# Kernel tuning notes

Measured on AMD Instinct MI355X. Metric: run time of the kernel, lower is better.

Reference implementation:

```python
import jax, jax.numpy as jnp
import numpy as np

B, A, D, H = 2048, 32, 128, 256

def setup_inputs() -> dict:
    key = jax.random.key(0)
    ks = jax.random.split(key, 12)
    s = lambda fan_in: 1.0 / np.sqrt(fan_in)
    return {
        "obs": jax.random.normal(ks[0], (B, A, D), dtype=jnp.float32),
        "act": jax.random.normal(ks[1], (B, A, 8), dtype=jnp.float32),
        "enc_W": jax.random.uniform(ks[2], (H, D), jnp.float32, -s(D), s(D)),
        "enc_b": jax.random.uniform(ks[3], (H,), jnp.float32, -s(D), s(D)),
        "fobs_W": jax.random.uniform(ks[4], (H, H), jnp.float32, -s(H), s(H)),
        "fobs_b": jax.random.uniform(ks[5], (H,), jnp.float32, -s(H), s(H)),
        "W_ih": jax.random.uniform(ks[6], (3 * H, H), jnp.float32, -s(H), s(H)),
        "b_ih": jax.random.uniform(ks[7], (3 * H,), jnp.float32, -s(H), s(H)),
        "W_hh": jax.random.uniform(ks[8], (3 * H, H), jnp.float32, -s(H), s(H)),
        "b_hh": jax.random.uniform(ks[9], (3 * H,), jnp.float32, -s(H), s(H)),
        "dec_W": jax.random.uniform(ks[10], (1, H), jnp.float32, -s(H), s(H)),
        "dec_b": jax.random.uniform(ks[11], (1,), jnp.float32, -s(H), s(H)),
    }

def _gru_cell(x, h, W_ih, b_ih, W_hh, b_hh):
    # torch.nn.GRUCell: gates stacked as [reset, update, new]
    gi = x @ W_ih.T + b_ih          # [N, 3H]
    gh = h @ W_hh.T + b_hh          # [N, 3H]
    i_r, i_z, i_n = jnp.split(gi, 3, axis=-1)
    h_r, h_z, h_n = jnp.split(gh, 3, axis=-1)
    r = jax.nn.sigmoid(i_r + h_r)
    z = jax.nn.sigmoid(i_z + h_z)
    n = jnp.tanh(i_n + r * h_n)
    return (1.0 - z) * n + z * h

def reference(obs, act, enc_W, enc_b, fobs_W, fobs_b, W_ih, b_ih, W_hh, b_hh, dec_W, dec_b):
    b, a, d = obs.shape
    x = obs.reshape(b * a, d)                         # [B*A, D]
    e = jax.nn.relu(x @ enc_W.T + enc_b)              # encoder + ReLU
    h = e @ fobs_W.T + fobs_b                         # h_out
    # k = 0: comm input is zeros
    h = _gru_cell(jnp.zeros_like(h), h, W_ih, b_ih, W_hh, b_hh)
    # k = 1: masked mean over other agents == (sum_j h_j - h_i) / n_agents
    hA = h.reshape(b, a, -1)                          # [B, A, H]
    c = (hA.sum(axis=1, keepdims=True) - hA) / a      # [B, A, H]
    h = _gru_cell(c.reshape(b * a, -1), h, W_ih, b_ih, W_hh, b_hh)
    return (h @ dec_W.T + dec_b).reshape(b, a, -1)    # [B, A, 1]
```

## Files before the change

### kernel.cpp

```cpp
#include <hip/hip_runtime.h>
#include <hip/hip_fp16.h>


#define NB   2048
#define NA   32
#define DIN  128
#define HID  256
#define SA   264
#define MROWS 64

typedef _Float16 half8  __attribute__((ext_vector_type(8)));
typedef float    float4v __attribute__((ext_vector_type(4)));

#define ENC_OFF    0
#define FOBS_OFF   32768
#define WIH_OFF    98304
#define WHH_OFF    294912
#define PREP_TOTAL 491520

__global__ void prep_weights(const float* __restrict__ encW, const float* __restrict__ fobsW,
                             const float* __restrict__ wih,  const float* __restrict__ whh,
                             _Float16* __restrict__ prep) {
    int F = blockIdx.x * 256 + threadIdx.x;
    if (F >= PREP_TOTAL) return;
    const float* src; int K, NT, local = F;
    if (F < FOBS_OFF)     { src = encW;  K = 128; NT = 16; }
    else if (F < WIH_OFF) { src = fobsW; K = 256; NT = 16; local = F - FOBS_OFF; }
    else if (F < WHH_OFF) { src = wih;   K = 256; NT = 48; local = F - WIH_OFF; }
    else                  { src = whh;   K = 256; NT = 48; local = F - WHH_OFF; }
    int j    = local & 7;
    int lane = (local >> 3) & 63;
    int t    = local >> 9;
    int nt   = t % NT;
    int ks   = t / NT;
    int col  = nt * 16 + (lane & 15);
    int k    = ks * 32 + ((lane >> 4) << 3) + j;
    prep[F] = (_Float16)src[col * K + k];
}

__device__ __forceinline__ float sigmoid_f(float x) {
    return 1.f / (1.f + __expf(-x));
}
__device__ __forceinline__ float tanh_f(float x) {
    return 1.f - 2.f / (__expf(2.f * x) + 1.f);
}

__device__ __forceinline__ half8 ldB(const _Float16* __restrict__ prepm, int NT, int nt, int ks,
                                     const float* __restrict__ raw, int K, int use_prep, int lane) {
    if (use_prep)
        return *(const half8*)(prepm + (((ks * NT + nt) * 64 + lane) << 3));
    half8 b;
    int l16 = lane & 15, kq = (lane >> 4) << 3;
    #pragma unroll
    for (int j = 0; j < 8; j++)
        b[j] = (_Float16)raw[(nt * 16 + l16) * K + ks * 32 + kq + j];
    return b;
}

__global__ __launch_bounds__(1024) void commnet_fused(
    const float* __restrict__ obs, const _Float16* __restrict__ prep,
    const float* __restrict__ enc_b, const float* __restrict__ fobs_b,
    const float* __restrict__ b_ih, const float* __restrict__ b_hh,
    const float* __restrict__ dec_W, const float* __restrict__ dec_b,
    float* __restrict__ out,
    const float* __restrict__ encW, const float* __restrict__ fobsW,
    const float* __restrict__ wih, const float* __restrict__ whh,
    int use_prep)
{
    const int b    = blockIdx.x;
    const int tid  = threadIdx.x;
    const int lane = tid & 63;
    const int nt   = tid >> 6;
    const int l16  = lane & 15;
    const int quad = lane >> 4;
    const int kq   = quad << 3;
    const int col  = nt * 16 + l16;

    __shared__ __align__(16) _Float16 sA[2][MROWS * SA];
    __shared__ __align__(16) float S[2][HID];
    __shared__ float Srow[MROWS];

    {
        const float* obsb = obs + (size_t)b * MROWS * DIN;
        int r   = tid >> 4;
        int off = (tid & 15) << 3;
        const float* src = obsb + r * DIN + off;
        float4v v0 = *(const float4v*)(src);
        float4v v1 = *(const float4v*)(src + 4);
        half8 hv;
        hv[0] = (_Float16)v0[0]; hv[1] = (_Float16)v0[1];
        hv[2] = (_Float16)v0[2]; hv[3] = (_Float16)v0[3];
        hv[4] = (_Float16)v1[0]; hv[5] = (_Float16)v1[1];
        hv[6] = (_Float16)v1[2]; hv[7] = (_Float16)v1[3];
        *(half8*)(&sA[0][r * SA + off]) = hv;
    }
    __syncthreads();

    {
        float4v acc[4];
        float4v z = {0.f, 0.f, 0.f, 0.f};
        acc[0] = z; acc[1] = z; acc[2] = z; acc[3] = z;
        #pragma unroll
        for (int ks = 0; ks < 4; ks++) {
            int kbase = ks * 32 + kq;
            half8 Af[4];
            #pragma unroll
            for (int mt = 0; mt < 4; mt++)
                Af[mt] = *(const half8*)(&sA[0][(mt * 16 + l16) * SA + kbase]);
            half8 b0 = ldB(prep + ENC_OFF, 16, nt, ks, encW, DIN, use_prep, lane);
            #pragma unroll
            for (int mt = 0; mt < 4; mt++)
                acc[mt] = __builtin_amdgcn_mfma_f32_16x16x32_f16(Af[mt], b0, acc[mt], 0, 0, 0);
        }
        float bb = enc_b[col];
        #pragma unroll
        for (int mt = 0; mt < 4; mt++)
            #pragma unroll
            for (int r = 0; r < 4; r++) {
                int row = mt * 16 + quad * 4 + r;
                sA[1][row * SA + col] = (_Float16)fmaxf(acc[mt][r] + bb, 0.f);
            }
    }
    __syncthreads();

    float4v hacc[4];
    {
        float4v z = {0.f, 0.f, 0.f, 0.f};
        hacc[0] = z; hacc[1] = z; hacc[2] = z; hacc[3] = z;
        #pragma unroll 2
        for (int ks = 0; ks < 8; ks++) {
            int kbase = ks * 32 + kq;
            half8 Af[4];
            #pragma unroll
            for (int mt = 0; mt < 4; mt++)
                Af[mt] = *(const half8*)(&sA[1][(mt * 16 + l16) * SA + kbase]);
            half8 b0 = ldB(prep + FOBS_OFF, 16, nt, ks, fobsW, HID, use_prep, lane);
            #pragma unroll
            for (int mt = 0; mt < 4; mt++)
                hacc[mt] = __builtin_amdgcn_mfma_f32_16x16x32_f16(Af[mt], b0, hacc[mt], 0, 0, 0);
        }
        float bb = fobs_b[col];
        #pragma unroll
        for (int mt = 0; mt < 4; mt++)
            #pragma unroll
            for (int r = 0; r < 4; r++) {
                int row = mt * 16 + quad * 4 + r;
                float h = hacc[mt][r] + bb;
                hacc[mt][r] = h;
                sA[0][row * SA + col] = (_Float16)h;
            }
    }
    __syncthreads();

    #pragma unroll 1
    for (int half = 0; half < 2; half++) {
        const int rb = half * 32;
        float4v aR[2], aZ[2], aN[2];
        float4v z = {0.f, 0.f, 0.f, 0.f};
        aR[0] = z; aR[1] = z; aZ[0] = z; aZ[1] = z; aN[0] = z; aN[1] = z;
        #pragma unroll 2
        for (int ks = 0; ks < 8; ks++) {
            const int kbase = ks * 32 + kq;
            half8 A0 = *(const half8*)(&sA[0][(rb + l16) * SA + kbase]);
            half8 A1 = *(const half8*)(&sA[0][(rb + 16 + l16) * SA + kbase]);
            half8 bR = ldB(prep + WHH_OFF, 48,  0 + nt, ks, whh, HID, use_prep, lane);
            half8 bZ = ldB(prep + WHH_OFF, 48, 16 + nt, ks, whh, HID, use_prep, lane);
            half8 bN = ldB(prep + WHH_OFF, 48, 32 + nt, ks, whh, HID, use_prep, lane);
            aR[0] = __builtin_amdgcn_mfma_f32_16x16x32_f16(A0, bR, aR[0], 0, 0, 0);
            aR[1] = __builtin_amdgcn_mfma_f32_16x16x32_f16(A1, bR, aR[1], 0, 0, 0);
            aZ[0] = __builtin_amdgcn_mfma_f32_16x16x32_f16(A0, bZ, aZ[0], 0, 0, 0);
            aZ[1] = __builtin_amdgcn_mfma_f32_16x16x32_f16(A1, bZ, aZ[1], 0, 0, 0);
            aN[0] = __builtin_amdgcn_mfma_f32_16x16x32_f16(A0, bN, aN[0], 0, 0, 0);
            aN[1] = __builtin_amdgcn_mfma_f32_16x16x32_f16(A1, bN, aN[1], 0, 0, 0);
        }
        float biR = b_ih[col],       bhR = b_hh[col];
        float biZ = b_ih[256 + col], bhZ = b_hh[256 + col];
        float biN = b_ih[512 + col], bhN = b_hh[512 + col];
        float psum = 0.f;
        #pragma unroll
        for (int mt = 0; mt < 2; mt++)
            #pragma unroll
            for (int r = 0; r < 4; r++) {
                int row = rb + mt * 16 + quad * 4 + r;
                float rg = sigmoid_f(biR + aR[mt][r] + bhR);
                float zg = sigmoid_f(biZ + aZ[mt][r] + bhZ);
                float ng = tanh_f(biN + rg * (aN[mt][r] + bhN));
                float hold = hacc[half * 2 + mt][r];
                float h1 = (1.f - zg) * ng + zg * hold;
                sA[1][row * SA + col] = (_Float16)h1;
                psum += h1;
            }
        psum += __shfl_xor(psum, 16);
        psum += __shfl_xor(psum, 32);
        if (lane < 16) S[half][nt * 16 + lane] = psum;
    }
    __syncthreads();

    {
        #pragma unroll
        for (int it = 0; it < 2; it++) {
            int i  = tid + it * 1024;
            int r  = i >> 5;
            int c8 = (i & 31) << 3;
            const float* Sp = &S[r >> 5][0];
            half8 hv = *(const half8*)(&sA[1][r * SA + c8]);
            float4v t0 = *(const float4v*)(Sp + c8);
            float4v t1 = *(const float4v*)(Sp + c8 + 4);
            half8 cv;
            cv[0] = (_Float16)((t0[0] - (float)hv[0]) * (1.f / 32.f));
            cv[1] = (_Float16)((t0[1] - (float)hv[1]) * (1.f / 32.f));
            cv[2] = (_Float16)((t0[2] - (float)hv[2]) * (1.f / 32.f));
            cv[3] = (_Float16)((t0[3] - (float)hv[3]) * (1.f / 32.f));
            cv[4] = (_Float16)((t1[0] - (float)hv[4]) * (1.f / 32.f));
            cv[5] = (_Float16)((t1[1] - (float)hv[5]) * (1.f / 32.f));
            cv[6] = (_Float16)((t1[2] - (float)hv[6]) * (1.f / 32.f));
            cv[7] = (_Float16)((t1[3] - (float)hv[7]) * (1.f / 32.f));
            *(half8*)(&sA[0][r * SA + c8]) = cv;
        }
        if (tid < MROWS) Srow[tid] = 0.f;
    }
    __syncthreads();

    #pragma unroll 1
    for (int half = 0; half < 2; half++) {
        const int rb = half * 32;
        float4v aR[2], aZ[2], aNi[2], aNh[2];
        float4v z = {0.f, 0.f, 0.f, 0.f};
        aR[0] = z; aR[1] = z; aZ[0] = z; aZ[1] = z;
        aNi[0] = z; aNi[1] = z; aNh[0] = z; aNh[1] = z;
        #pragma unroll 1
        for (int ks = 0; ks < 8; ks++) {
            const int kbase = ks * 32 + kq;
            {
                half8 C0 = *(const half8*)(&sA[0][(rb + l16) * SA + kbase]);
                half8 C1 = *(const half8*)(&sA[0][(rb + 16 + l16) * SA + kbase]);
                half8 bR = ldB(prep + WIH_OFF, 48,  0 + nt, ks, wih, HID, use_prep, lane);
                half8 bZ = ldB(prep + WIH_OFF, 48, 16 + nt, ks, wih, HID, use_prep, lane);
                half8 bN = ldB(prep + WIH_OFF, 48, 32 + nt, ks, wih, HID, use_prep, lane);
                aR[0]  = __builtin_amdgcn_mfma_f32_16x16x32_f16(C0, bR, aR[0], 0, 0, 0);
                aR[1]  = __builtin_amdgcn_mfma_f32_16x16x32_f16(C1, bR, aR[1], 0, 0, 0);
                aZ[0]  = __builtin_amdgcn_mfma_f32_16x16x32_f16(C0, bZ, aZ[0], 0, 0, 0);
                aZ[1]  = __builtin_amdgcn_mfma_f32_16x16x32_f16(C1, bZ, aZ[1], 0, 0, 0);
                aNi[0] = __builtin_amdgcn_mfma_f32_16x16x32_f16(C0, bN, aNi[0], 0, 0, 0);
                aNi[1] = __builtin_amdgcn_mfma_f32_16x16x32_f16(C1, bN, aNi[1], 0, 0, 0);
            }
            {
                half8 H0 = *(const half8*)(&sA[1][(rb + l16) * SA + kbase]);
                half8 H1 = *(const half8*)(&sA[1][(rb + 16 + l16) * SA + kbase]);
                half8 bR = ldB(prep + WHH_OFF, 48,  0 + nt, ks, whh, HID, use_prep, lane);
                half8 bZ = ldB(prep + WHH_OFF, 48, 16 + nt, ks, whh, HID, use_prep, lane);
                half8 bN = ldB(prep + WHH_OFF, 48, 32 + nt, ks, whh, HID, use_prep, lane);
                aR[0]  = __builtin_amdgcn_mfma_f32_16x16x32_f16(H0, bR, aR[0], 0, 0, 0);
                aR[1]  = __builtin_amdgcn_mfma_f32_16x16x32_f16(H1, bR, aR[1], 0, 0, 0);
                aZ[0]  = __builtin_amdgcn_mfma_f32_16x16x32_f16(H0, bZ, aZ[0], 0, 0, 0);
                aZ[1]  = __builtin_amdgcn_mfma_f32_16x16x32_f16(H1, bZ, aZ[1], 0, 0, 0);
                aNh[0] = __builtin_amdgcn_mfma_f32_16x16x32_f16(H0, bN, aNh[0], 0, 0, 0);
                aNh[1] = __builtin_amdgcn_mfma_f32_16x16x32_f16(H1, bN, aNh[1], 0, 0, 0);
            }
        }

        float biR = b_ih[col],       bhR = b_hh[col];
        float biZ = b_ih[256 + col], bhZ = b_hh[256 + col];
        float biN = b_ih[512 + col], bhN = b_hh[512 + col];
        float dw  = dec_W[col];
        float p[2][4];
        #pragma unroll
        for (int mt = 0; mt < 2; mt++)
            #pragma unroll
            for (int r = 0; r < 4; r++) {
                int row = rb + mt * 16 + quad * 4 + r;
                float rg = sigmoid_f(aR[mt][r] + biR + bhR);
                float zg = sigmoid_f(aZ[mt][r] + biZ + bhZ);
                float ng = tanh_f((aNi[mt][r] + biN) + rg * (aNh[mt][r] + bhN));
                float h1v = (float)sA[1][row * SA + col];
                float h2 = (1.f - zg) * ng + zg * h1v;
                p[mt][r] = h2 * dw;
            }
        #pragma unroll
        for (int m = 1; m <= 8; m <<= 1) {
            #pragma unroll
            for (int mt = 0; mt < 2; mt++)
                #pragma unroll
                for (int r = 0; r < 4; r++)
                    p[mt][r] += __shfl_xor(p[mt][r], m);
        }
        if (l16 == 0) {
            #pragma unroll
            for (int mt = 0; mt < 2; mt++)
                #pragma unroll
                for (int r = 0; r < 4; r++)
                    atomicAdd(&Srow[rb + mt * 16 + quad * 4 + r], p[mt][r]);
        }
    }
    __syncthreads();
    if (tid < MROWS) out[(size_t)b * MROWS + tid] = Srow[tid] + dec_b[0];
}

extern "C" void kernel_launch(void* const* d_in, const int* in_sizes, int n_in,
                              void* d_out, int out_size, void* d_ws, size_t ws_size,
                              hipStream_t stream) {
    const float* obs   = (const float*)d_in[0];
    const float* encW  = (const float*)d_in[2];
    const float* encb  = (const float*)d_in[3];
    const float* fobsW = (const float*)d_in[4];
    const float* fobsb = (const float*)d_in[5];
    const float* wih   = (const float*)d_in[6];
    const float* bih   = (const float*)d_in[7];
    const float* whh   = (const float*)d_in[8];
    const float* bhh   = (const float*)d_in[9];
    const float* decW  = (const float*)d_in[10];
    const float* decb  = (const float*)d_in[11];
    float* out = (float*)d_out;

    _Float16* prep = (_Float16*)d_ws;
    int use_prep = (ws_size >= (size_t)PREP_TOTAL * sizeof(_Float16)) ? 1 : 0;
    if (use_prep) {
        prep_weights<<<(PREP_TOTAL + 255) / 256, 256, 0, stream>>>(encW, fobsW, wih, whh, prep);
    }
    commnet_fused<<<NB / 2, 1024, 0, stream>>>(obs, prep, encb, fobsb, bih, bhh, decW, decb, out,
                                               encW, fobsW, wih, whh, use_prep);
}
```

Baseline: 236.6 us.

## Fold mean-field comm into combined GRU weights to drop second-step input GEMM

```diff
diff --git a/kernel.cpp b/kernel.cpp
--- a/kernel.cpp
+++ b/kernel.cpp
@@ -14,8 +14,9 @@
 
 #define ENC_OFF    0
 #define FOBS_OFF   32768
-#define WIH_OFF    98304
-#define WHH_OFF    294912
+#define WIHN_OFF   98304
+#define WHH_OFF    163840
+#define COMB_OFF   360448
 #define PREP_TOTAL 491520
 
 __global__ void prep_weights(const float* __restrict__ encW, const float* __restrict__ fobsW,
@@ -23,19 +24,25 @@
                              _Float16* __restrict__ prep) {
     int F = blockIdx.x * 256 + threadIdx.x;
     if (F >= PREP_TOTAL) return;
-    const float* src; int K, NT, local = F;
-    if (F < FOBS_OFF)     { src = encW;  K = 128; NT = 16; }
-    else if (F < WIH_OFF) { src = fobsW; K = 256; NT = 16; local = F - FOBS_OFF; }
-    else if (F < WHH_OFF) { src = wih;   K = 256; NT = 48; local = F - WIH_OFF; }
-    else                  { src = whh;   K = 256; NT = 48; local = F - WHH_OFF; }
+    const float* srcA; const float* srcB = nullptr;
+    int K, NT, local, rowoff = 0; float scA = 1.f, scB = 0.f;
+    if (F < FOBS_OFF)      { srcA = encW;  K = 128; NT = 16; local = F; }
+    else if (F < WIHN_OFF) { srcA = fobsW; K = 256; NT = 16; local = F - FOBS_OFF; }
+    else if (F < WHH_OFF)  { srcA = wih;   K = 256; NT = 16; local = F - WIHN_OFF;
+                             rowoff = 512; scA = -0.03125f; }
+    else if (F < COMB_OFF) { srcA = whh;   K = 256; NT = 48; local = F - WHH_OFF; }
+    else                   { srcA = whh; srcB = wih; K = 256; NT = 32;
+                             local = F - COMB_OFF; scB = -0.03125f; }
     int j    = local & 7;
     int lane = (local >> 3) & 63;
     int t    = local >> 9;
     int nt   = t % NT;
     int ks   = t / NT;
-    int col  = nt * 16 + (lane & 15);
+    int row  = rowoff + nt * 16 + (lane & 15);
     int k    = ks * 32 + ((lane >> 4) << 3) + j;
-    prep[F] = (_Float16)src[col * K + k];
+    float v  = srcA[row * K + k] * scA;
+    if (srcB) v += srcB[row * K + k] * scB;
+    prep[F] = (_Float16)v;
 }
 
 __device__ __forceinline__ float sigmoid_f(float x) {
@@ -46,14 +53,20 @@
 }
 
 __device__ __forceinline__ half8 ldB(const _Float16* __restrict__ prepm, int NT, int nt, int ks,
-                                     const float* __restrict__ raw, int K, int use_prep, int lane) {
-    if (use_prep)
-        return *(const half8*)(prepm + (((ks * NT + nt) * 64 + lane) << 3));
-    half8 b;
-    int l16 = lane & 15, kq = (lane >> 4) << 3;
+                                     int lane) {
+    return *(const half8*)(prepm + (((ks * NT + nt) * 64 + lane) << 3));
+}
+__device__ __forceinline__ half8 ldBraw(const float* __restrict__ rawA, float scA,
+                                        const float* __restrict__ rawB, float scB,
+                                        int rowoff, int K, int nt, int ks, int lane) {
+    half8 b; int l16 = lane & 15, kq = (lane >> 4) << 3;
+    int row = rowoff + nt * 16 + l16;
     #pragma unroll
-    for (int j = 0; j < 8; j++)
-        b[j] = (_Float16)raw[(nt * 16 + l16) * K + ks * 32 + kq + j];
+    for (int j = 0; j < 8; j++) {
+        float v = rawA[row * K + ks * 32 + kq + j] * scA;
+        if (rawB) v += rawB[row * K + ks * 32 + kq + j] * scB;
+        b[j] = (_Float16)v;
+    }
     return b;
 }
 
@@ -77,7 +90,8 @@
     const int col  = nt * 16 + l16;
 
     __shared__ __align__(16) _Float16 sA[2][MROWS * SA];
-    __shared__ __align__(16) float S[2][HID];
+    __shared__ __align__(16) float Scol[2][HID];
+    __shared__ __align__(16) float ep[2][3 * HID];
     __shared__ float Srow[MROWS];
 
     {
@@ -107,7 +121,8 @@
             #pragma unroll
             for (int mt = 0; mt < 4; mt++)
                 Af[mt] = *(const half8*)(&sA[0][(mt * 16 + l16) * SA + kbase]);
-            half8 b0 = ldB(prep + ENC_OFF, 16, nt, ks, encW, DIN, use_prep, lane);
+            half8 b0 = use_prep ? ldB(prep + ENC_OFF, 16, nt, ks, lane)
+                                : ldBraw(encW, 1.f, nullptr, 0.f, 0, DIN, nt, ks, lane);
             #pragma unroll
             for (int mt = 0; mt < 4; mt++)
                 acc[mt] = __builtin_amdgcn_mfma_f32_16x16x32_f16(Af[mt], b0, acc[mt], 0, 0, 0);
@@ -134,7 +149,8 @@
             #pragma unroll
             for (int mt = 0; mt < 4; mt++)
                 Af[mt] = *(const half8*)(&sA[1][(mt * 16 + l16) * SA + kbase]);
-            half8 b0 = ldB(prep + FOBS_OFF, 16, nt, ks, fobsW, HID, use_prep, lane);
+            half8 b0 = use_prep ? ldB(prep + FOBS_OFF, 16, nt, ks, lane)
+                                : ldBraw(fobsW, 1.f, nullptr, 0.f, 0, HID, nt, ks, lane);
             #pragma unroll
             for (int mt = 0; mt < 4; mt++)
                 hacc[mt] = __builtin_amdgcn_mfma_f32_16x16x32_f16(Af[mt], b0, hacc[mt], 0, 0, 0);
@@ -163,9 +179,12 @@
             const int kbase = ks * 32 + kq;
             half8 A0 = *(const half8*)(&sA[0][(rb + l16) * SA + kbase]);
             half8 A1 = *(const half8*)(&sA[0][(rb + 16 + l16) * SA + kbase]);
-            half8 bR = ldB(prep + WHH_OFF, 48,  0 + nt, ks, whh, HID, use_prep, lane);
-            half8 bZ = ldB(prep + WHH_OFF, 48, 16 + nt, ks, whh, HID, use_prep, lane);
-            half8 bN = ldB(prep + WHH_OFF, 48, 32 + nt, ks, whh, HID, use_prep, lane);
+            half8 bR = use_prep ? ldB(prep + WHH_OFF, 48,  0 + nt, ks, lane)
+                                : ldBraw(whh, 1.f, nullptr, 0.f, 0, HID,  0 + nt, ks, lane);
+            half8 bZ = use_prep ? ldB(prep + WHH_OFF, 48, 16 + nt, ks, lane)
+                                : ldBraw(whh, 1.f, nullptr, 0.f, 0, HID, 16 + nt, ks, lane);
+            half8 bN = use_prep ? ldB(prep + WHH_OFF, 48, 32 + nt, ks, lane)
+                                : ldBraw(whh, 1.f, nullptr, 0.f, 0, HID, 32 + nt, ks, lane);
             aR[0] = __builtin_amdgcn_mfma_f32_16x16x32_f16(A0, bR, aR[0], 0, 0, 0);
             aR[1] = __builtin_amdgcn_mfma_f32_16x16x32_f16(A1, bR, aR[1], 0, 0, 0);
             aZ[0] = __builtin_amdgcn_mfma_f32_16x16x32_f16(A0, bZ, aZ[0], 0, 0, 0);
@@ -192,30 +211,57 @@
             }
         psum += __shfl_xor(psum, 16);
         psum += __shfl_xor(psum, 32);
-        if (lane < 16) S[half][nt * 16 + lane] = psum;
+        if (lane < 16) Scol[half][nt * 16 + lane] = psum;
     }
     __syncthreads();
 
     {
-        #pragma unroll
-        for (int it = 0; it < 2; it++) {
-            int i  = tid + it * 1024;
-            int r  = i >> 5;
-            int c8 = (i & 31) << 3;
-            const float* Sp = &S[r >> 5][0];
-            half8 hv = *(const half8*)(&sA[1][r * SA + c8]);
-            float4v t0 = *(const float4v*)(Sp + c8);
-            float4v t1 = *(const float4v*)(Sp + c8 + 4);
-            half8 cv;
-            cv[0] = (_Float16)((t0[0] - (float)hv[0]) * (1.f / 32.f));
-            cv[1] = (_Float16)((t0[1] - (float)hv[1]) * (1.f / 32.f));
-            cv[2] = (_Float16)((t0[2] - (float)hv[2]) * (1.f / 32.f));
-            cv[3] = (_Float16)((t0[3] - (float)hv[3]) * (1.f / 32.f));
-            cv[4] = (_Float16)((t1[0] - (float)hv[4]) * (1.f / 32.f));
-            cv[5] = (_Float16)((t1[1] - (float)hv[5]) * (1.f / 32.f));
-            cv[6] = (_Float16)((t1[2] - (float)hv[6]) * (1.f / 32.f));
-            cv[7] = (_Float16)((t1[3] - (float)hv[7]) * (1.f / 32.f));
-            *(half8*)(&sA[0][r * SA + c8]) = cv;
+        float4v g[3];
+        float4v zz = {0.f, 0.f, 0.f, 0.f};
+        g[0] = zz; g[1] = zz; g[2] = zz;
+        #pragma unroll 1
+        for (int ks = 0; ks < 8; ks++) {
+            const int kbase = ks * 32 + kq;
+            half8 aS;
+            #pragma unroll
+            for (int j = 0; j < 8; j++) aS[j] = (_Float16)0.f;
+            if (l16 < 2) {
+                const float* Sp = &Scol[l16][kbase];
+                float4v s0 = *(const float4v*)(Sp);
+                float4v s1 = *(const float4v*)(Sp + 4);
+                aS[0] = (_Float16)s0[0]; aS[1] = (_Float16)s0[1];
+                aS[2] = (_Float16)s0[2]; aS[3] = (_Float16)s0[3];
+                aS[4] = (_Float16)s1[0]; aS[5] = (_Float16)s1[1];
+                aS[6] = (_Float16)s1[2]; aS[7] = (_Float16)s1[3];
+            }
+            #pragma unroll
+            for (int i = 0; i < 3; i++) {
+                int t3 = 3 * nt + i;
+                half8 bw;
+                if (use_prep) {
+                    if (t3 < 32) {
+                        half8 x = ldB(prep + WHH_OFF,  48, t3, ks, lane);
+                        half8 y = ldB(prep + COMB_OFF, 32, t3, ks, lane);
+                        bw = x - y;
+                    } else {
+                        half8 x = ldB(prep + WIHN_OFF, 16, t3 - 32, ks, lane);
+                        bw = half8{} - x;
+                    }
+                } else {
+                    bw = ldBraw(wih, 0.03125f, nullptr, 0.f, 0, HID, t3, ks, lane);
+                }
+                g[i] = __builtin_amdgcn_mfma_f32_16x16x32_f16(aS, bw, g[i], 0, 0, 0);
+            }
+        }
+        if (quad == 0) {
+            #pragma unroll
+            for (int i = 0; i < 3; i++) {
+                int j = (3 * nt + i) * 16 + l16;
+                float bi = b_ih[j];
+                float bh = (j < 512) ? b_hh[j] : 0.f;
+                ep[0][j] = g[i][0] + bi + bh;
+                ep[1][j] = g[i][1] + bi + bh;
+            }
         }
         if (tid < MROWS) Srow[tid] = 0.f;
     }
@@ -228,40 +274,33 @@
         float4v z = {0.f, 0.f, 0.f, 0.f};
         aR[0] = z; aR[1] = z; aZ[0] = z; aZ[1] = z;
         aNi[0] = z; aNi[1] = z; aNh[0] = z; aNh[1] = z;
-        #pragma unroll 1
+        #pragma unroll 2
         for (int ks = 0; ks < 8; ks++) {
             const int kbase = ks * 32 + kq;
-            {
-                half8 C0 = *(const half8*)(&sA[0][(rb + l16) * SA + kbase]);
-                half8 C1 = *(const half8*)(&sA[0][(rb + 16 + l16) * SA + kbase]);
-                half8 bR = ldB(prep + WIH_OFF, 48,  0 + nt, ks, wih, HID, use_prep, lane);
-                half8 bZ = ldB(prep + WIH_OFF, 48, 16 + nt, ks, wih, HID, use_prep, lane);
-                half8 bN = ldB(prep + WIH_OFF, 48, 32 + nt, ks, wih, HID, use_prep, lane);
-                aR[0]  = __builtin_amdgcn_mfma_f32_16x16x32_f16(C0, bR, aR[0], 0, 0, 0);
-                aR[1]  = __builtin_amdgcn_mfma_f32_16x16x32_f16(C1, bR, aR[1], 0, 0, 0);
-                aZ[0]  = __builtin_amdgcn_mfma_f32_16x16x32_f16(C0, bZ, aZ[0], 0, 0, 0);
-                aZ[1]  = __builtin_amdgcn_mfma_f32_16x16x32_f16(C1, bZ, aZ[1], 0, 0, 0);
-                aNi[0] = __builtin_amdgcn_mfma_f32_16x16x32_f16(C0, bN, aNi[0], 0, 0, 0);
-                aNi[1] = __builtin_amdgcn_mfma_f32_16x16x32_f16(C1, bN, aNi[1], 0, 0, 0);
-            }
-            {
-                half8 H0 = *(const half8*)(&sA[1][(rb + l16) * SA + kbase]);
-                half8 H1 = *(const half8*)(&sA[1][(rb + 16 + l16) * SA + kbase]);
-                half8 bR = ldB(prep + WHH_OFF, 48,  0 + nt, ks, whh, HID, use_prep, lane);
-                half8 bZ = ldB(prep + WHH_OFF, 48, 16 + nt, ks, whh, HID, use_prep, lane);
-                half8 bN = ldB(prep + WHH_OFF, 48, 32 + nt, ks, whh, HID, use_prep, lane);
-                aR[0]  = __builtin_amdgcn_mfma_f32_16x16x32_f16(H0, bR, aR[0], 0, 0, 0);
-                aR[1]  = __builtin_amdgcn_mfma_f32_16x16x32_f16(H1, bR, aR[1], 0, 0, 0);
-                aZ[0]  = __builtin_amdgcn_mfma_f32_16x16x32_f16(H0, bZ, aZ[0], 0, 0, 0);
-                aZ[1]  = __builtin_amdgcn_mfma_f32_16x16x32_f16(H1, bZ, aZ[1], 0, 0, 0);
-                aNh[0] = __builtin_amdgcn_mfma_f32_16x16x32_f16(H0, bN, aNh[0], 0, 0, 0);
-                aNh[1] = __builtin_amdgcn_mfma_f32_16x16x32_f16(H1, bN, aNh[1], 0, 0, 0);
-            }
-        }
-
-        float biR = b_ih[col],       bhR = b_hh[col];
-        float biZ = b_ih[256 + col], bhZ = b_hh[256 + col];
-        float biN = b_ih[512 + col], bhN = b_hh[512 + col];
+            half8 H0 = *(const half8*)(&sA[1][(rb + l16) * SA + kbase]);
+            half8 H1 = *(const half8*)(&sA[1][(rb + 16 + l16) * SA + kbase]);
+            half8 bR  = use_prep ? ldB(prep + COMB_OFF, 32,  0 + nt, ks, lane)
+                                 : ldBraw(whh, 1.f, wih, -0.03125f, 0, HID,  0 + nt, ks, lane);
+            half8 bZ  = use_prep ? ldB(prep + COMB_OFF, 32, 16 + nt, ks, lane)
+                                 : ldBraw(whh, 1.f, wih, -0.03125f, 0, HID, 16 + nt, ks, lane);
+            half8 bNi = use_prep ? ldB(prep + WIHN_OFF, 16, nt, ks, lane)
+                                 : ldBraw(wih, -0.03125f, nullptr, 0.f, 512, HID, nt, ks, lane);
+            half8 bNh = use_prep ? ldB(prep + WHH_OFF, 48, 32 + nt, ks, lane)
+                                 : ldBraw(whh, 1.f, nullptr, 0.f, 0, HID, 32 + nt, ks, lane);
+            aR[0]  = __builtin_amdgcn_mfma_f32_16x16x32_f16(H0, bR,  aR[0],  0, 0, 0);
+            aR[1]  = __builtin_amdgcn_mfma_f32_16x16x32_f16(H1, bR,  aR[1],  0, 0, 0);
+            aZ[0]  = __builtin_amdgcn_mfma_f32_16x16x32_f16(H0, bZ,  aZ[0],  0, 0, 0);
+            aZ[1]  = __builtin_amdgcn_mfma_f32_16x16x32_f16(H1, bZ,  aZ[1],  0, 0, 0);
+            aNi[0] = __builtin_amdgcn_mfma_f32_16x16x32_f16(H0, bNi, aNi[0], 0, 0, 0);
+            aNi[1] = __builtin_amdgcn_mfma_f32_16x16x32_f16(H1, bNi, aNi[1], 0, 0, 0);
+            aNh[0] = __builtin_amdgcn_mfma_f32_16x16x32_f16(H0, bNh, aNh[0], 0, 0, 0);
+            aNh[1] = __builtin_amdgcn_mfma_f32_16x16x32_f16(H1, bNh, aNh[1], 0, 0, 0);
+        }
+
+        float epR = ep[half][col];
+        float epZ = ep[half][256 + col];
+        float epN = ep[half][512 + col];
+        float bhN = b_hh[512 + col];
         float dw  = dec_W[col];
         float p[2][4];
         #pragma unroll
@@ -269,9 +308,9 @@
             #pragma unroll
             for (int r = 0; r < 4; r++) {
                 int row = rb + mt * 16 + quad * 4 + r;
-                float rg = sigmoid_f(aR[mt][r] + biR + bhR);
-                float zg = sigmoid_f(aZ[mt][r] + biZ + bhZ);
-                float ng = tanh_f((aNi[mt][r] + biN) + rg * (aNh[mt][r] + bhN));
+                float rg = sigmoid_f(aR[mt][r] + epR);
+                float zg = sigmoid_f(aZ[mt][r] + epZ);
+                float ng = tanh_f(aNi[mt][r] + epN + rg * (aNh[mt][r] + bhN));
                 float h1v = (float)sA[1][row * SA + col];
                 float h2 = (1.f - zg) * ng + zg * h1v;
                 p[mt][r] = h2 * dw;
```

Measured after the change: 255.8 us. 1.08x slower.
